# Kernel optimization log

Hardware: AMD Instinct MI355X
Metric: run time of the kernel (lower is better)

The kernel has to match this reference:

```python
import jax, jax.numpy as jnp
import numpy as np

B, H, W, C_IN = 16, 32, 32, 2048
C_PROJ = 2048          # hard-coded Conv2D filters in the module
D_Q = 512              # queries last dim
A = 64                 # num_attributes


def setup_inputs() -> dict:
    key = jax.random.key(0)
    ks = jax.random.split(key, 8)
    s = lambda fan_in: 1.0 / np.sqrt(fan_in)
    return {
        "queries": jax.random.normal(ks[0], (B, C_PROJ, D_Q), jnp.float32),
        "features": jax.random.normal(ks[1], (B, H, W, C_IN), jnp.float32),
        # Dense(num_attributes) on queries
        "Wq": jax.random.normal(ks[2], (D_Q, A), jnp.float32) * s(D_Q),
        "bq": jnp.zeros((A,), jnp.float32),
        # Conv2D 1x1 -> 2048 (feature_transform)
        "Wf": jax.random.normal(ks[3], (C_IN, C_PROJ), jnp.float32) * s(C_IN),
        "bf": jnp.zeros((C_PROJ,), jnp.float32),
        # Conv2D 1x1 -> 2048 (feature_transform1)
        "Wf1": jax.random.normal(ks[4], (C_IN, C_PROJ), jnp.float32) * s(C_IN),
        "bf1": jnpp if False else jnp.zeros((C_PROJ,), jnp.float32),
    }


def reference(queries, features, Wq, bq, Wf, bf, Wf1, bf1):
    # Q: [B, C_PROJ, A]
    Q = jnp.einsum("bcd,da->bca", queries, Wq) + bq
    # 1x1 convs are per-pixel linear maps: [B, H, W, C_PROJ]
    F = jnp.einsum("bhwc,cf->bhwf", features, Wf) + bf
    S = jnp.einsum("bhwc,cf->bhwf", features, Wf1) + bf1
    b, h, w, c = F.shape
    F_new = F.reshape(b, h * w, c)                      # [B, HW, C]
    scale = 1.0 / jnp.sqrt(jnp.float32(A))
    # scores: [B, HW, A]; softmax over attribute axis
    attn = jax.nn.softmax(jnp.einsum("bnc,bca->bna", F_new, Q) * scale, axis=-1)
    attention_map = attn.reshape(b, h, w, A)
    S_flat = S.reshape(b, h * w, c)                     # [B, HW, C]
    # readout: S^T @ attn -> [B, C, A]
    out = jnp.einsum("bnc,bna->bca", S_flat, attn)
    return attention_map, out
```

## Files before the change

### kernel.cpp

```cpp
#include <hip/hip_runtime.h>
#include <math.h>


#define CCH 2048
#define HWD 1024
#define BAD 1024
#define DQD 512
#define NA  64

typedef __attribute__((ext_vector_type(8))) short bf16x8;
typedef __attribute__((ext_vector_type(4))) float f32x4;
typedef __attribute__((ext_vector_type(4))) unsigned short us4;
typedef __attribute__((ext_vector_type(8))) unsigned short us8;

__device__ __forceinline__ unsigned short bfhi(float v) {
    return (unsigned short)(__float_as_uint(v) >> 16);
}
__device__ __forceinline__ float bfres(float v) {
    return v - __uint_as_float(__float_as_uint(v) & 0xffff0000u);
}
__device__ __forceinline__ float bf2f(unsigned short h) {
    return __uint_as_float(((unsigned)h) << 16);
}

__global__ __launch_bounds__(256) void k_convWq(const float* __restrict__ Wq,
    unsigned short* __restrict__ hi, unsigned short* __restrict__ lo)
{
    __shared__ float t[64][65];
    const int tid = threadIdx.x;
    const int k0 = blockIdx.x * 64;
#pragma unroll
    for (int r = 0; r < 4; ++r) {
        int kr = (tid >> 4) + r * 16;
        int cc = (tid & 15) * 4;
        float4 v = *(const float4*)&Wq[(size_t)(k0 + kr) * NA + cc];
        t[kr][cc] = v.x; t[kr][cc + 1] = v.y; t[kr][cc + 2] = v.z; t[kr][cc + 3] = v.w;
    }
    __syncthreads();
#pragma unroll
    for (int r = 0; r < 2; ++r) {
        int a = (tid >> 3) + r * 32;
        int g = tid & 7;
        us8 h8, l8;
#pragma unroll
        for (int j = 0; j < 8; ++j) {
            float v = t[g * 8 + j][a];
            h8[j] = bfhi(v); l8[j] = bfhi(bfres(v));
        }
        *(us8*)&hi[(size_t)a * DQD + k0 + g * 8] = h8;
        *(us8*)&lo[(size_t)a * DQD + k0 + g * 8] = l8;
    }
}

template <int EPI>
__global__ __launch_bounds__(256) void k_gemm_A32(
    const float* __restrict__ A,
    const unsigned short* __restrict__ Bh, const unsigned short* __restrict__ Bl,
    const float* __restrict__ bias,
    unsigned short* __restrict__ Oh, unsigned short* __restrict__ Ol,
    int K, int ldb)
{
    __shared__ unsigned short AsH[4][64][8], AsL[4][64][8], BsH[4][64][8], BsL[4][64][8];
    const int tid = threadIdx.x;
    const int m0 = blockIdx.x * 64, gy = blockIdx.y;
    const int w = tid >> 6, l = tid & 63, lr = l & 15, lg = l >> 4;
    const int sm = tid >> 2, sk = tid & 3, kq = sk * 4;

    const float* pA = A + (size_t)(m0 + sm) * K;
    const unsigned short* pBh = Bh + (size_t)(gy * 64 + sm) * ldb + sk * 8;
    const unsigned short* pBl = Bl + (size_t)(gy * 64 + sm) * ldb + sk * 8;

    f32x4 acc[4] = {{0.f,0.f,0.f,0.f},{0.f,0.f,0.f,0.f},{0.f,0.f,0.f,0.f},{0.f,0.f,0.f,0.f}};

    for (int k0 = 0; k0 < K; k0 += 32) {
        float4 a0 = *(const float4*)&pA[k0 + kq];
        float4 a1 = *(const float4*)&pA[k0 + 16 + kq];
        uint4 vbh = *(const uint4*)pBh; uint4 vbl = *(const uint4*)pBl;
        pBh += 32; pBl += 32;
        us4 h0, l0, h1, l1;
        float a0r[4] = {a0.x, a0.y, a0.z, a0.w}, a1r[4] = {a1.x, a1.y, a1.z, a1.w};
#pragma unroll
        for (int j = 0; j < 4; ++j) {
            h0[j] = bfhi(a0r[j]); l0[j] = bfhi(bfres(a0r[j]));
            h1[j] = bfhi(a1r[j]); l1[j] = bfhi(bfres(a1r[j]));
        }
        __syncthreads();
        *(us4*)&AsH[kq >> 3][sm][kq & 7] = h0;
        *(us4*)&AsL[kq >> 3][sm][kq & 7] = l0;
        *(us4*)&AsH[2 + (kq >> 3)][sm][kq & 7] = h1;
        *(us4*)&AsL[2 + (kq >> 3)][sm][kq & 7] = l1;
        *(uint4*)&BsH[sk][sm][0] = vbh;
        *(uint4*)&BsL[sk][sm][0] = vbl;
        __syncthreads();
        bf16x8 afh = *(const bf16x8*)&AsH[lg][w * 16 + lr][0];
        bf16x8 afl = *(const bf16x8*)&AsL[lg][w * 16 + lr][0];
#pragma unroll
        for (int nt = 0; nt < 4; ++nt) {
            bf16x8 bfh = *(const bf16x8*)&BsH[lg][nt * 16 + lr][0];
            bf16x8 bfl = *(const bf16x8*)&BsL[lg][nt * 16 + lr][0];
            acc[nt] = __builtin_amdgcn_mfma_f32_16x16x32_bf16(afh, bfh, acc[nt], 0, 0, 0);
            acc[nt] = __builtin_amdgcn_mfma_f32_16x16x32_bf16(afh, bfl, acc[nt], 0, 0, 0);
            acc[nt] = __builtin_amdgcn_mfma_f32_16x16x32_bf16(afl, bfh, acc[nt], 0, 0, 0);
        }
    }

    const int mrow0 = m0 + w * 16 + lg * 4;
    if (EPI == 0) {
#pragma unroll
        for (int nt = 0; nt < 4; ++nt) {
            int nn = gy * 64 + nt * 16 + lr;
            us4 h, lo;
#pragma unroll
            for (int j = 0; j < 4; ++j) {
                float v = acc[nt][j];
                h[j] = bfhi(v); lo[j] = bfhi(bfres(v));
            }
            *(us4*)&Oh[(size_t)nn * CCH + mrow0] = h;
            *(us4*)&Ol[(size_t)nn * CCH + mrow0] = lo;
        }
    } else {
        const int b = mrow0 >> 11, cp = mrow0 & 2047;
#pragma unroll
        for (int nt = 0; nt < 4; ++nt) {
            int nloc = nt * 16 + lr;
            float bb = bias[nloc];
            int row = b * 64 + nloc;
            us4 h, lo;
#pragma unroll
            for (int j = 0; j < 4; ++j) {
                float v = acc[nt][j] + bb;
                h[j] = bfhi(v); lo[j] = bfhi(bfres(v));
            }
            *(us4*)&Oh[(size_t)row * CCH + cp] = h;
            *(us4*)&Ol[(size_t)row * CCH + cp] = lo;
        }
    }
}

__global__ __launch_bounds__(256) void k_bq(const unsigned short* __restrict__ QTh,
    const unsigned short* __restrict__ QTl, const float* __restrict__ bf,
    float* __restrict__ bQ)
{
    const int row = blockIdx.x, tid = threadIdx.x;
    us8 h = *(const us8*)(QTh + (size_t)row * CCH + tid * 8);
    us8 l = *(const us8*)(QTl + (size_t)row * CCH + tid * 8);
    float s = 0.f;
#pragma unroll
    for (int j = 0; j < 8; ++j)
        s = fmaf(bf2f(h[j]) + bf2f(l[j]), bf[tid * 8 + j], s);
#pragma unroll
    for (int off = 1; off < 64; off <<= 1) s += __shfl_xor(s, off);
    __shared__ float ps[4];
    if ((tid & 63) == 0) ps[tid >> 6] = s;
    __syncthreads();
    if (tid == 0) bQ[row] = ps[0] + ps[1] + ps[2] + ps[3];
}

__global__ __launch_bounds__(256) void k_scores(
    const float* __restrict__ feat,
    const unsigned short* __restrict__ FQh, const unsigned short* __restrict__ FQl,
    const float* __restrict__ bQ, float* __restrict__ attn,
    unsigned short* __restrict__ ATh, unsigned short* __restrict__ ATl)
{
    __shared__ unsigned short AsH[4][64][8], AsL[4][64][8], BsH[4][64][8], BsL[4][64][8];
    const int tid = threadIdx.x;
    const int b = blockIdx.y, n0 = blockIdx.x * 64;
    const int w = tid >> 6, l = tid & 63, lr = l & 15, lg = l >> 4;
    const int sm = tid >> 2, sk = tid & 3, kq = sk * 4;

    const float* fb = feat + ((size_t)b * HWD + n0) * CCH;
    const unsigned short* pBh = FQh + (size_t)(b * 64 + sm) * CCH + sk * 8;
    const unsigned short* pBl = FQl + (size_t)(b * 64 + sm) * CCH + sk * 8;

    f32x4 acc[4] = {{0.f,0.f,0.f,0.f},{0.f,0.f,0.f,0.f},{0.f,0.f,0.f,0.f},{0.f,0.f,0.f,0.f}};

    for (int k0 = 0; k0 < CCH; k0 += 32) {
        float4 a0 = *(const float4*)&fb[(size_t)sm * CCH + k0 + kq];
        float4 a1 = *(const float4*)&fb[(size_t)sm * CCH + k0 + 16 + kq];
        uint4 vbh = *(const uint4*)pBh; uint4 vbl = *(const uint4*)pBl;
        pBh += 32; pBl += 32;
        us4 h0, l0, h1, l1;
        float a0r[4] = {a0.x, a0.y, a0.z, a0.w}, a1r[4] = {a1.x, a1.y, a1.z, a1.w};
#pragma unroll
        for (int j = 0; j < 4; ++j) {
            h0[j] = bfhi(a0r[j]); l0[j] = bfhi(bfres(a0r[j]));
            h1[j] = bfhi(a1r[j]); l1[j] = bfhi(bfres(a1r[j]));
        }
        __syncthreads();
        *(us4*)&AsH[kq >> 3][sm][kq & 7] = h0;
        *(us4*)&AsL[kq >> 3][sm][kq & 7] = l0;
        *(us4*)&AsH[2 + (kq >> 3)][sm][kq & 7] = h1;
        *(us4*)&AsL[2 + (kq >> 3)][sm][kq & 7] = l1;
        *(uint4*)&BsH[sk][sm][0] = vbh;
        *(uint4*)&BsL[sk][sm][0] = vbl;
        __syncthreads();
        bf16x8 afh = *(const bf16x8*)&AsH[lg][w * 16 + lr][0];
        bf16x8 afl = *(const bf16x8*)&AsL[lg][w * 16 + lr][0];
#pragma unroll
        for (int nt = 0; nt < 4; ++nt) {
            bf16x8 bfh = *(const bf16x8*)&BsH[lg][nt * 16 + lr][0];
            bf16x8 bfl = *(const bf16x8*)&BsL[lg][nt * 16 + lr][0];
            acc[nt] = __builtin_amdgcn_mfma_f32_16x16x32_bf16(afh, bfh, acc[nt], 0, 0, 0);
            acc[nt] = __builtin_amdgcn_mfma_f32_16x16x32_bf16(afh, bfl, acc[nt], 0, 0, 0);
            acc[nt] = __builtin_amdgcn_mfma_f32_16x16x32_bf16(afl, bfh, acc[nt], 0, 0, 0);
        }
    }

    float bq4[4];
#pragma unroll
    for (int nt = 0; nt < 4; ++nt) bq4[nt] = bQ[b * NA + nt * 16 + lr];
#pragma unroll
    for (int j = 0; j < 4; ++j) {
        float v[4];
#pragma unroll
        for (int nt = 0; nt < 4; ++nt) v[nt] = (acc[nt][j] + bq4[nt]) * 0.125f;
        float m = fmaxf(fmaxf(v[0], v[1]), fmaxf(v[2], v[3]));
        m = fmaxf(m, __shfl_xor(m, 1));
        m = fmaxf(m, __shfl_xor(m, 2));
        m = fmaxf(m, __shfl_xor(m, 4));
        m = fmaxf(m, __shfl_xor(m, 8));
        float e[4], s = 0.f;
#pragma unroll
        for (int nt = 0; nt < 4; ++nt) { e[nt] = expf(v[nt] - m); s += e[nt]; }
        s += __shfl_xor(s, 1);
        s += __shfl_xor(s, 2);
        s += __shfl_xor(s, 4);
        s += __shfl_xor(s, 8);
        float inv = 1.f / s;
        const int nr = n0 + w * 16 + lg * 4 + j;
#pragma unroll
        for (int nt = 0; nt < 4; ++nt) {
            float av = e[nt] * inv;
            attn[((size_t)b * HWD + nr) * NA + nt * 16 + lr] = av;
            size_t trow = (size_t)(b * 64 + nt * 16 + lr) * HWD + nr;
            ATh[trow] = bfhi(av);
            ATl[trow] = bfhi(bfres(av));
        }
    }
}

__global__ __launch_bounds__(256) void k_lsum1(const float* __restrict__ attn,
                                               float* __restrict__ part)
{
    const int g = blockIdx.x, b = blockIdx.y;
    const int a = threadIdx.x & 63, q = threadIdx.x >> 6;
    float s = 0.f;
#pragma unroll 4
    for (int n = g * 64 + q * 16; n < g * 64 + q * 16 + 16; ++n)
        s += attn[((size_t)b * HWD + n) * NA + a];
    __shared__ float p[4][64];
    p[q][a] = s;
    __syncthreads();
    if (q == 0) part[(size_t)g * BAD + b * NA + a] = p[0][a] + p[1][a] + p[2][a] + p[3][a];
}

__global__ __launch_bounds__(64) void k_lsum2(const float* __restrict__ part,
                                              float* __restrict__ L)
{
    int ba = blockIdx.x * 64 + threadIdx.x;
    float s = 0.f;
#pragma unroll
    for (int g = 0; g < 16; ++g) s += part[(size_t)g * BAD + ba];
    L[ba] = s;
}

template <int EPI>
__global__ __launch_bounds__(256) void k_gemm_T(
    const float* __restrict__ G,
    const unsigned short* __restrict__ Bh, const unsigned short* __restrict__ Bl,
    unsigned short* __restrict__ Oh, unsigned short* __restrict__ Ol,
    float* __restrict__ Ofp, const float* __restrict__ bias, const float* __restrict__ Lv,
    int K, int ldg, int ldb, long gslab)
{
    __shared__ float At[2048];
    __shared__ unsigned short BsH[4][64][8], BsL[4][64][8];
    const int tid = threadIdx.x;
    const int m0 = blockIdx.x * 64, gy = blockIdx.y;
    const int w = tid >> 6, l = tid & 63, lr = l & 15, lg = l >> 4;
    const int sm = tid >> 2, sk = tid & 3;
    const int kr = tid >> 3, c8 = (tid & 7) * 8;
    const int wkey = (kr >> 3) << 4;
    const int acol = ((w ^ lg) << 4) | lr;

    const float* Gb = G + (size_t)gy * gslab;
    const unsigned short* pBh = Bh + (size_t)(gy * 64 + sm) * ldb + sk * 8;
    const unsigned short* pBl = Bl + (size_t)(gy * 64 + sm) * ldb + sk * 8;

    f32x4 acc[4] = {{0.f,0.f,0.f,0.f},{0.f,0.f,0.f,0.f},{0.f,0.f,0.f,0.f},{0.f,0.f,0.f,0.f}};

    for (int k0 = 0; k0 < K; k0 += 32) {
        float4 g0 = *(const float4*)&Gb[(size_t)(k0 + kr) * ldg + m0 + c8];
        float4 g1 = *(const float4*)&Gb[(size_t)(k0 + kr) * ldg + m0 + c8 + 4];
        uint4 vbh = *(const uint4*)pBh; uint4 vbl = *(const uint4*)pBl;
        pBh += 32; pBl += 32;
        __syncthreads();
        *(float4*)&At[kr * 64 + (c8 ^ wkey)] = g0;
        *(float4*)&At[kr * 64 + (c8 ^ wkey) + 4] = g1;
        *(uint4*)&BsH[sk][sm][0] = vbh;
        *(uint4*)&BsL[sk][sm][0] = vbl;
        __syncthreads();
        bf16x8 afh, afl;
#pragma unroll
        for (int j = 0; j < 8; ++j) {
            float v = At[(lg * 8 + j) * 64 + acol];
            afh[j] = (short)bfhi(v);
            afl[j] = (short)bfhi(bfres(v));
        }
#pragma unroll
        for (int nt = 0; nt < 4; ++nt) {
            bf16x8 bfh = *(const bf16x8*)&BsH[lg][nt * 16 + lr][0];
            bf16x8 bfl = *(const bf16x8*)&BsL[lg][nt * 16 + lr][0];
            acc[nt] = __builtin_amdgcn_mfma_f32_16x16x32_bf16(afh, bfh, acc[nt], 0, 0, 0);
            acc[nt] = __builtin_amdgcn_mfma_f32_16x16x32_bf16(afh, bfl, acc[nt], 0, 0, 0);
            acc[nt] = __builtin_amdgcn_mfma_f32_16x16x32_bf16(afl, bfh, acc[nt], 0, 0, 0);
        }
    }

    const int mrow0 = m0 + w * 16 + lg * 4;
    if (EPI == 0) {
#pragma unroll
        for (int nt = 0; nt < 4; ++nt) {
            int nn = gy * 64 + nt * 16 + lr;
            us4 h, lo;
#pragma unroll
            for (int j = 0; j < 4; ++j) {
                float v = acc[nt][j];
                h[j] = bfhi(v); lo[j] = bfhi(bfres(v));
            }
            *(us4*)&Oh[(size_t)nn * CCH + mrow0] = h;
            *(us4*)&Ol[(size_t)nn * CCH + mrow0] = lo;
        }
    } else {
        float bv[4];
#pragma unroll
        for (int j = 0; j < 4; ++j) bv[j] = bias[mrow0 + j];
#pragma unroll
        for (int nt = 0; nt < 4; ++nt) {
            int nn = gy * 64 + nt * 16 + lr;
            float lb = Lv[nn];
            size_t base = (size_t)(nn >> 6) * (CCH * NA) + (size_t)(nn & 63);
#pragma unroll
            for (int j = 0; j < 4; ++j)
                Ofp[base + (size_t)(mrow0 + j) * NA] = fmaf(bv[j], lb, acc[nt][j]);
        }
    }
}

extern "C" void kernel_launch(void* const* d_in, const int* in_sizes, int n_in,
                              void* d_out, int out_size, void* d_ws, size_t ws_size,
                              hipStream_t stream)
{
    (void)in_sizes; (void)n_in; (void)out_size; (void)ws_size;
    const float* queries  = (const float*)d_in[0];
    const float* features = (const float*)d_in[1];
    const float* Wq  = (const float*)d_in[2];
    const float* bq  = (const float*)d_in[3];
    const float* Wf  = (const float*)d_in[4];
    const float* bf  = (const float*)d_in[5];
    const float* Wf1 = (const float*)d_in[6];
    const float* bf1 = (const float*)d_in[7];
    float* out = (float*)d_out;
    char*  W   = (char*)d_ws;

    unsigned short* QTh = (unsigned short*)(W);
    unsigned short* QTl = (unsigned short*)(W + (4u << 20));
    unsigned short* FQh = (unsigned short*)(W + (8u << 20));
    unsigned short* FQl = (unsigned short*)(W + (12u << 20));
    unsigned short* WqTh = (unsigned short*)(W + (16u << 20));
    unsigned short* WqTl = (unsigned short*)(W + (16u << 20) + (64u << 10));
    float* bQ   = (float*)(W + (16u << 20) + (128u << 10));
    float* L    = (float*)(W + (16u << 20) + (128u << 10) + 4096);
    float* part = (float*)(W + (16u << 20) + (128u << 10) + 8192);
    unsigned short* ATh = QTh;
    unsigned short* ATl = (unsigned short*)(W + (2u << 20));
    unsigned short* TTh = FQh;
    unsigned short* TTl = FQl;

    float* attn = out;
    float* outm = out + 1048576;

    k_convWq<<<dim3(8), 256, 0, stream>>>(Wq, WqTh, WqTl);
    k_gemm_A32<1><<<dim3(512, 1), 256, 0, stream>>>(queries, WqTh, WqTl, bq, QTh, QTl,
                                                    DQD, DQD);
    k_bq<<<dim3(1024), 256, 0, stream>>>(QTh, QTl, bf, bQ);
    k_gemm_A32<0><<<dim3(32, 16), 256, 0, stream>>>(Wf, QTh, QTl, nullptr, FQh, FQl,
                                                    CCH, CCH);
    k_scores<<<dim3(16, 16), 256, 0, stream>>>(features, FQh, FQl, bQ, attn, ATh, ATl);
    k_lsum1<<<dim3(16, 16), 256, 0, stream>>>(attn, part);
    k_lsum2<<<dim3(16), 64, 0, stream>>>(part, L);
    k_gemm_T<0><<<dim3(32, 16), 256, 0, stream>>>(features, ATh, ATl, TTh, TTl,
                                                  nullptr, nullptr, nullptr,
                                                  HWD, CCH, HWD, (long)HWD * CCH);
    k_gemm_T<1><<<dim3(32, 16), 256, 0, stream>>>(Wf1, TTh, TTl, nullptr, nullptr,
                                                  outm, bf1, L,
                                                  CCH, CCH, CCH, 0L);
}
```

Measured before the change: 489.1 us.

## Double-buffer LDS tiles and load A fragments directly into registers in GEMMs

```diff
diff --git a/kernel.cpp b/kernel.cpp
--- a/kernel.cpp
+++ b/kernel.cpp
@@ -22,6 +22,15 @@
 __device__ __forceinline__ float bf2f(unsigned short h) {
     return __uint_as_float(((unsigned)h) << 16);
 }
+__device__ __forceinline__ void cvt8(const float4& a0, const float4& a1,
+                                     bf16x8& h, bf16x8& l) {
+    float ar[8] = {a0.x, a0.y, a0.z, a0.w, a1.x, a1.y, a1.z, a1.w};
+#pragma unroll
+    for (int j = 0; j < 8; ++j) {
+        h[j] = (short)bfhi(ar[j]);
+        l[j] = (short)bfhi(bfres(ar[j]));
+    }
+}
 
 __global__ __launch_bounds__(256) void k_convWq(const float* __restrict__ Wq,
     unsigned short* __restrict__ hi, unsigned short* __restrict__ lo)
@@ -53,55 +62,60 @@
 }
 
 template <int EPI>
-__global__ __launch_bounds__(256) void k_gemm_A32(
+__global__ __launch_bounds__(256) void k_gemm_w(
     const float* __restrict__ A,
     const unsigned short* __restrict__ Bh, const unsigned short* __restrict__ Bl,
     const float* __restrict__ bias,
     unsigned short* __restrict__ Oh, unsigned short* __restrict__ Ol,
     int K, int ldb)
 {
-    __shared__ unsigned short AsH[4][64][8], AsL[4][64][8], BsH[4][64][8], BsL[4][64][8];
+    __shared__ unsigned short BsH[2][4][64][8], BsL[2][4][64][8];
     const int tid = threadIdx.x;
     const int m0 = blockIdx.x * 64, gy = blockIdx.y;
     const int w = tid >> 6, l = tid & 63, lr = l & 15, lg = l >> 4;
-    const int sm = tid >> 2, sk = tid & 3, kq = sk * 4;
-
-    const float* pA = A + (size_t)(m0 + sm) * K;
+    const int sm = tid >> 2, sk = tid & 3;
+
+    const float* pA = A + (size_t)(m0 + w * 16 + lr) * K + lg * 8;
     const unsigned short* pBh = Bh + (size_t)(gy * 64 + sm) * ldb + sk * 8;
     const unsigned short* pBl = Bl + (size_t)(gy * 64 + sm) * ldb + sk * 8;
 
     f32x4 acc[4] = {{0.f,0.f,0.f,0.f},{0.f,0.f,0.f,0.f},{0.f,0.f,0.f,0.f},{0.f,0.f,0.f,0.f}};
 
+    float4 a0 = *(const float4*)&pA[0];
+    float4 a1 = *(const float4*)&pA[4];
+    {
+        uint4 vh = *(const uint4*)pBh, vl = *(const uint4*)pBl;
+        pBh += 32; pBl += 32;
+        *(uint4*)&BsH[0][sk][sm][0] = vh;
+        *(uint4*)&BsL[0][sk][sm][0] = vl;
+    }
+    int buf = 0;
     for (int k0 = 0; k0 < K; k0 += 32) {
-        float4 a0 = *(const float4*)&pA[k0 + kq];
-        float4 a1 = *(const float4*)&pA[k0 + 16 + kq];
-        uint4 vbh = *(const uint4*)pBh; uint4 vbl = *(const uint4*)pBl;
-        pBh += 32; pBl += 32;
-        us4 h0, l0, h1, l1;
-        float a0r[4] = {a0.x, a0.y, a0.z, a0.w}, a1r[4] = {a1.x, a1.y, a1.z, a1.w};
-#pragma unroll
-        for (int j = 0; j < 4; ++j) {
-            h0[j] = bfhi(a0r[j]); l0[j] = bfhi(bfres(a0r[j]));
-            h1[j] = bfhi(a1r[j]); l1[j] = bfhi(bfres(a1r[j]));
+        const bool notlast = (k0 + 32 < K);
+        float4 na0, na1; uint4 nh, nl;
+        if (notlast) {
+            na0 = *(const float4*)&pA[k0 + 32];
+            na1 = *(const float4*)&pA[k0 + 36];
+            nh = *(const uint4*)pBh; nl = *(const uint4*)pBl;
+            pBh += 32; pBl += 32;
         }
         __syncthreads();
-        *(us4*)&AsH[kq >> 3][sm][kq & 7] = h0;
-        *(us4*)&AsL[kq >> 3][sm][kq & 7] = l0;
-        *(us4*)&AsH[2 + (kq >> 3)][sm][kq & 7] = h1;
-        *(us4*)&AsL[2 + (kq >> 3)][sm][kq & 7] = l1;
-        *(uint4*)&BsH[sk][sm][0] = vbh;
-        *(uint4*)&BsL[sk][sm][0] = vbl;
-        __syncthreads();
-        bf16x8 afh = *(const bf16x8*)&AsH[lg][w * 16 + lr][0];
-        bf16x8 afl = *(const bf16x8*)&AsL[lg][w * 16 + lr][0];
-#pragma unroll
-        for (int nt = 0; nt < 4; ++nt) {
-            bf16x8 bfh = *(const bf16x8*)&BsH[lg][nt * 16 + lr][0];
-            bf16x8 bfl = *(const bf16x8*)&BsL[lg][nt * 16 + lr][0];
+        bf16x8 afh, afl;
+        cvt8(a0, a1, afh, afl);
+#pragma unroll
+        for (int nt = 0; nt < 4; ++nt) {
+            bf16x8 bfh = *(const bf16x8*)&BsH[buf][lg][nt * 16 + lr][0];
+            bf16x8 bfl = *(const bf16x8*)&BsL[buf][lg][nt * 16 + lr][0];
             acc[nt] = __builtin_amdgcn_mfma_f32_16x16x32_bf16(afh, bfh, acc[nt], 0, 0, 0);
             acc[nt] = __builtin_amdgcn_mfma_f32_16x16x32_bf16(afh, bfl, acc[nt], 0, 0, 0);
             acc[nt] = __builtin_amdgcn_mfma_f32_16x16x32_bf16(afl, bfh, acc[nt], 0, 0, 0);
         }
+        if (notlast) {
+            *(uint4*)&BsH[buf ^ 1][sk][sm][0] = nh;
+            *(uint4*)&BsL[buf ^ 1][sk][sm][0] = nl;
+            a0 = na0; a1 = na1;
+        }
+        buf ^= 1;
     }
 
     const int mrow0 = m0 + w * 16 + lg * 4;
@@ -162,53 +176,59 @@
     const float* __restrict__ bQ, float* __restrict__ attn,
     unsigned short* __restrict__ ATh, unsigned short* __restrict__ ATl)
 {
-    __shared__ unsigned short AsH[4][64][8], AsL[4][64][8], BsH[4][64][8], BsL[4][64][8];
+    __shared__ unsigned short BsH[2][4][64][8], BsL[2][4][64][8];
     const int tid = threadIdx.x;
-    const int b = blockIdx.y, n0 = blockIdx.x * 64;
+    const int b = blockIdx.x, n0 = blockIdx.y * 64;
     const int w = tid >> 6, l = tid & 63, lr = l & 15, lg = l >> 4;
-    const int sm = tid >> 2, sk = tid & 3, kq = sk * 4;
-
-    const float* fb = feat + ((size_t)b * HWD + n0) * CCH;
+    const int sm = tid >> 2, sk = tid & 3;
+
+    const float* pA = feat + ((size_t)b * HWD + n0 + w * 16 + lr) * CCH + lg * 8;
     const unsigned short* pBh = FQh + (size_t)(b * 64 + sm) * CCH + sk * 8;
     const unsigned short* pBl = FQl + (size_t)(b * 64 + sm) * CCH + sk * 8;
 
     f32x4 acc[4] = {{0.f,0.f,0.f,0.f},{0.f,0.f,0.f,0.f},{0.f,0.f,0.f,0.f},{0.f,0.f,0.f,0.f}};
 
+    float4 a0 = *(const float4*)&pA[0];
+    float4 a1 = *(const float4*)&pA[4];
+    {
+        uint4 vh = *(const uint4*)pBh, vl = *(const uint4*)pBl;
+        pBh += 32; pBl += 32;
+        *(uint4*)&BsH[0][sk][sm][0] = vh;
+        *(uint4*)&BsL[0][sk][sm][0] = vl;
+    }
+    int buf = 0;
     for (int k0 = 0; k0 < CCH; k0 += 32) {
-        float4 a0 = *(const float4*)&fb[(size_t)sm * CCH + k0 + kq];
-        float4 a1 = *(const float4*)&fb[(size_t)sm * CCH + k0 + 16 + kq];
-        uint4 vbh = *(const uint4*)pBh; uint4 vbl = *(const uint4*)pBl;
-        pBh += 32; pBl += 32;
-        us4 h0, l0, h1, l1;
-        float a0r[4] = {a0.x, a0.y, a0.z, a0.w}, a1r[4] = {a1.x, a1.y, a1.z, a1.w};
-#pragma unroll
-        for (int j = 0; j < 4; ++j) {
-            h0[j] = bfhi(a0r[j]); l0[j] = bfhi(bfres(a0r[j]));
-            h1[j] = bfhi(a1r[j]); l1[j] = bfhi(bfres(a1r[j]));
+        const bool notlast = (k0 + 32 < CCH);
+        float4 na0, na1; uint4 nh, nl;
+        if (notlast) {
+            na0 = *(const float4*)&pA[k0 + 32];
+            na1 = *(const float4*)&pA[k0 + 36];
+            nh = *(const uint4*)pBh; nl = *(const uint4*)pBl;
+            pBh += 32; pBl += 32;
         }
         __syncthreads();
-        *(us4*)&AsH[kq >> 3][sm][kq & 7] = h0;
-        *(us4*)&AsL[kq >> 3][sm][kq & 7] = l0;
-        *(us4*)&AsH[2 + (kq >> 3)][sm][kq & 7] = h1;
-        *(us4*)&AsL[2 + (kq >> 3)][sm][kq & 7] = l1;
-        *(uint4*)&BsH[sk][sm][0] = vbh;
-        *(uint4*)&BsL[sk][sm][0] = vbl;
-        __syncthreads();
-        bf16x8 afh = *(const bf16x8*)&AsH[lg][w * 16 + lr][0];
-        bf16x8 afl = *(const bf16x8*)&AsL[lg][w * 16 + lr][0];
-#pragma unroll
-        for (int nt = 0; nt < 4; ++nt) {
-            bf16x8 bfh = *(const bf16x8*)&BsH[lg][nt * 16 + lr][0];
-            bf16x8 bfl = *(const bf16x8*)&BsL[lg][nt * 16 + lr][0];
+        bf16x8 afh, afl;
+        cvt8(a0, a1, afh, afl);
+#pragma unroll
+        for (int nt = 0; nt < 4; ++nt) {
+            bf16x8 bfh = *(const bf16x8*)&BsH[buf][lg][nt * 16 + lr][0];
+            bf16x8 bfl = *(const bf16x8*)&BsL[buf][lg][nt * 16 + lr][0];
             acc[nt] = __builtin_amdgcn_mfma_f32_16x16x32_bf16(afh, bfh, acc[nt], 0, 0, 0);
             acc[nt] = __builtin_amdgcn_mfma_f32_16x16x32_bf16(afh, bfl, acc[nt], 0, 0, 0);
             acc[nt] = __builtin_amdgcn_mfma_f32_16x16x32_bf16(afl, bfh, acc[nt], 0, 0, 0);
         }
+        if (notlast) {
+            *(uint4*)&BsH[buf ^ 1][sk][sm][0] = nh;
+            *(uint4*)&BsL[buf ^ 1][sk][sm][0] = nl;
+            a0 = na0; a1 = na1;
+        }
+        buf ^= 1;
     }
 
     float bq4[4];
 #pragma unroll
     for (int nt = 0; nt < 4; ++nt) bq4[nt] = bQ[b * NA + nt * 16 + lr];
+    float pv[4][4];
 #pragma unroll
     for (int j = 0; j < 4; ++j) {
         float v[4];
@@ -231,11 +251,21 @@
 #pragma unroll
         for (int nt = 0; nt < 4; ++nt) {
             float av = e[nt] * inv;
+            pv[j][nt] = av;
             attn[((size_t)b * HWD + nr) * NA + nt * 16 + lr] = av;
-            size_t trow = (size_t)(b * 64 + nt * 16 + lr) * HWD + nr;
-            ATh[trow] = bfhi(av);
-            ATl[trow] = bfhi(bfres(av));
-        }
+        }
+    }
+#pragma unroll
+    for (int nt = 0; nt < 4; ++nt) {
+        us4 h, lo;
+#pragma unroll
+        for (int j = 0; j < 4; ++j) {
+            h[j] = bfhi(pv[j][nt]);
+            lo[j] = bfhi(bfres(pv[j][nt]));
+        }
+        size_t ro = (size_t)(b * 64 + nt * 16 + lr) * HWD + n0 + w * 16 + lg * 4;
+        *(us4*)&ATh[ro] = h;
+        *(us4*)&ATl[ro] = lo;
     }
 }
 
@@ -272,48 +302,66 @@
     float* __restrict__ Ofp, const float* __restrict__ bias, const float* __restrict__ Lv,
     int K, int ldg, int ldb, long gslab)
 {
-    __shared__ float At[2048];
-    __shared__ unsigned short BsH[4][64][8], BsL[4][64][8];
+    __shared__ float At[2][2048];
+    __shared__ unsigned short BsH[2][4][64][8], BsL[2][4][64][8];
     const int tid = threadIdx.x;
-    const int m0 = blockIdx.x * 64, gy = blockIdx.y;
+    const int m0 = (EPI == 0 ? blockIdx.y : blockIdx.x) * 64;
+    const int gy = (EPI == 0 ? blockIdx.x : blockIdx.y);
     const int w = tid >> 6, l = tid & 63, lr = l & 15, lg = l >> 4;
     const int sm = tid >> 2, sk = tid & 3;
     const int kr = tid >> 3, c8 = (tid & 7) * 8;
     const int wkey = (kr >> 3) << 4;
     const int acol = ((w ^ lg) << 4) | lr;
 
-    const float* Gb = G + (size_t)gy * gslab;
+    const float* Gb = G + (size_t)gy * gslab + m0 + c8;
     const unsigned short* pBh = Bh + (size_t)(gy * 64 + sm) * ldb + sk * 8;
     const unsigned short* pBl = Bl + (size_t)(gy * 64 + sm) * ldb + sk * 8;
 
     f32x4 acc[4] = {{0.f,0.f,0.f,0.f},{0.f,0.f,0.f,0.f},{0.f,0.f,0.f,0.f},{0.f,0.f,0.f,0.f}};
 
+    {
+        float4 g0 = *(const float4*)&Gb[(size_t)kr * ldg];
+        float4 g1 = *(const float4*)&Gb[(size_t)kr * ldg + 4];
+        uint4 vh = *(const uint4*)pBh, vl = *(const uint4*)pBl;
+        pBh += 32; pBl += 32;
+        *(float4*)&At[0][kr * 64 + (c8 ^ wkey)] = g0;
+        *(float4*)&At[0][kr * 64 + (c8 ^ wkey) + 4] = g1;
+        *(uint4*)&BsH[0][sk][sm][0] = vh;
+        *(uint4*)&BsL[0][sk][sm][0] = vl;
+    }
+    int buf = 0;
     for (int k0 = 0; k0 < K; k0 += 32) {
-        float4 g0 = *(const float4*)&Gb[(size_t)(k0 + kr) * ldg + m0 + c8];
-        float4 g1 = *(const float4*)&Gb[(size_t)(k0 + kr) * ldg + m0 + c8 + 4];
-        uint4 vbh = *(const uint4*)pBh; uint4 vbl = *(const uint4*)pBl;
-        pBh += 32; pBl += 32;
-        __syncthreads();
-        *(float4*)&At[kr * 64 + (c8 ^ wkey)] = g0;
-        *(float4*)&At[kr * 64 + (c8 ^ wkey) + 4] = g1;
-        *(uint4*)&BsH[sk][sm][0] = vbh;
-        *(uint4*)&BsL[sk][sm][0] = vbl;
+        const bool notlast = (k0 + 32 < K);
+        float4 ng0, ng1; uint4 nh, nl;
+        if (notlast) {
+            ng0 = *(const float4*)&Gb[(size_t)(k0 + 32 + kr) * ldg];
+            ng1 = *(const float4*)&Gb[(size_t)(k0 + 32 + kr) * ldg + 4];
+            nh = *(const uint4*)pBh; nl = *(const uint4*)pBl;
+            pBh += 32; pBl += 32;
+        }
         __syncthreads();
         bf16x8 afh, afl;
 #pragma unroll
         for (int j = 0; j < 8; ++j) {
-            float v = At[(lg * 8 + j) * 64 + acol];
+            float v = At[buf][(lg * 8 + j) * 64 + acol];
             afh[j] = (short)bfhi(v);
             afl[j] = (short)bfhi(bfres(v));
         }
 #pragma unroll
         for (int nt = 0; nt < 4; ++nt) {
-            bf16x8 bfh = *(const bf16x8*)&BsH[lg][nt * 16 + lr][0];
-            bf16x8 bfl = *(const bf16x8*)&BsL[lg][nt * 16 + lr][0];
+            bf16x8 bfh = *(const bf16x8*)&BsH[buf][lg][nt * 16 + lr][0];
+            bf16x8 bfl = *(const bf16x8*)&BsL[buf][lg][nt * 16 + lr][0];
             acc[nt] = __builtin_amdgcn_mfma_f32_16x16x32_bf16(afh, bfh, acc[nt], 0, 0, 0);
             acc[nt] = __builtin_amdgcn_mfma_f32_16x16x32_bf16(afh, bfl, acc[nt], 0, 0, 0);
             acc[nt] = __builtin_amdgcn_mfma_f32_16x16x32_bf16(afl, bfh, acc[nt], 0, 0, 0);
         }
+        if (notlast) {
+            *(float4*)&At[buf ^ 1][kr * 64 + (c8 ^ wkey)] = ng0;
+            *(float4*)&At[buf ^ 1][kr * 64 + (c8 ^ wkey) + 4] = ng1;
+            *(uint4*)&BsH[buf ^ 1][sk][sm][0] = nh;
+            *(uint4*)&BsL[buf ^ 1][sk][sm][0] = nl;
+        }
+        buf ^= 1;
     }
 
     const int mrow0 = m0 + w * 16 + lg * 4;
@@ -380,15 +428,15 @@
     float* outm = out + 1048576;
 
     k_convWq<<<dim3(8), 256, 0, stream>>>(Wq, WqTh, WqTl);
-    k_gemm_A32<1><<<dim3(512, 1), 256, 0, stream>>>(queries, WqTh, WqTl, bq, QTh, QTl,
-                                                    DQD, DQD);
+    k_gemm_w<1><<<dim3(512, 1), 256, 0, stream>>>(queries, WqTh, WqTl, bq, QTh, QTl,
+                                                  DQD, DQD);
     k_bq<<<dim3(1024), 256, 0, stream>>>(QTh, QTl, bf, bQ);
-    k_gemm_A32<0><<<dim3(32, 16), 256, 0, stream>>>(Wf, QTh, QTl, nullptr, FQh, FQl,
-                                                    CCH, CCH);
+    k_gemm_w<0><<<dim3(32, 16), 256, 0, stream>>>(Wf, QTh, QTl, nullptr, FQh, FQl,
+                                                  CCH, CCH);
     k_scores<<<dim3(16, 16), 256, 0, stream>>>(features, FQh, FQl, bQ, attn, ATh, ATl);
     k_lsum1<<<dim3(16, 16), 256, 0, stream>>>(attn, part);
     k_lsum2<<<dim3(16), 64, 0, stream>>>(part, L);
-    k_gemm_T<0><<<dim3(32, 16), 256, 0, stream>>>(features, ATh, ATl, TTh, TTl,
+    k_gemm_T<0><<<dim3(16, 32), 256, 0, stream>>>(features, ATh, ATl, TTh, TTl,
                                                   nullptr, nullptr, nullptr,
                                                   HWD, CCH, HWD, (long)HWD * CCH);
     k_gemm_T<1><<<dim3(32, 16), 256, 0, stream>>>(Wf1, TTh, TTl, nullptr, nullptr,
```

New measurement: 425.5 us. -13.0%, faster.
